# Performance work log

Hardware: AMD Instinct MI355X
Metric: run time of the kernel (lower is better)

## Reference

```python
import jax, jax.numpy as jnp
import numpy as np

N, C, E, K = 50000, 128, 640000, 40  # nodes, feat dim, edges, classes
EPS = 1e-5


def setup_inputs() -> dict:
    key = jax.random.key(0)
    ks = jax.random.split(key, 8)
    s = 1.0 / np.sqrt(C)
    return {
        "x": jax.random.normal(ks[0], (N, C), jnp.float32),
        "edge_index": jax.random.randint(ks[1], (2, E), 0, N, dtype=jnp.int32),
        "W_conv": jax.random.normal(ks[2], (C, C), jnp.float32) * s,
        "b_conv": jnp.zeros((C,), jnp.float32),
        "gamma": jnp.ones((C,), jnp.float32),
        "beta": jnp.zeros((C,), jnp.float32),
        "W_fc": jax.random.normal(ks[3], (C, K), jnp.float32) * s,
        "b_fc": jnp.zeros((K,), jnp.float32),
    }


def reference(x, edge_index, W_conv, b_conv, gamma, beta, W_fc, b_fc):
    n = x.shape[0]
    loops = jnp.arange(n, dtype=edge_index.dtype)
    src = jnp.concatenate([edge_index[0], loops])  # add self-loops (PyG default)
    dst = jnp.concatenate([edge_index[1], loops])
    # symmetric normalization: deg^{-1/2}[src] * deg^{-1/2}[dst]
    deg = jax.ops.segment_sum(jnp.ones_like(dst, jnp.float32), dst, num_segments=n)
    dinv = jax.lax.rsqrt(jnp.maximum(deg, 1.0))  # deg >= 1 with self-loops
    norm = dinv[src] * dinv[dst]  # [E+N]
    h = x @ W_conv  # [N, C] transform before propagate (GCNConv)
    agg = jax.ops.segment_sum(h[src] * norm[:, None], dst, num_segments=n) + b_conv
    a = jax.nn.relu(agg) * x  # dropout = identity (eval mode); elementwise mul with residual
    mu = jnp.mean(a, axis=-1, keepdims=True)
    var = jnp.mean((a - mu) ** 2, axis=-1, keepdims=True)
    ln = (a - mu) * jax.lax.rsqrt(var + EPS) * gamma + beta
    return (ln + x) @ W_fc + b_fc
```

## Files before the change

### kernel.cpp

```cpp
#include <hip/hip_runtime.h>

#define C_DIM 128
#define EPS 1e-5f
#define DEG_CAP 64

typedef __attribute__((ext_vector_type(8))) short short8;
typedef __attribute__((ext_vector_type(4))) float f32x4;

__device__ __forceinline__ unsigned bf16rn(float f) {
    unsigned u = __float_as_uint(f);
    return (u + 0x7fffu + ((u >> 16) & 1u)) >> 16;
}
__device__ __forceinline__ unsigned pack_bf16(float lo, float hi) {
    return bf16rn(lo) | (bf16rn(hi) << 16);
}
__device__ __forceinline__ float blo(unsigned u) { return __uint_as_float(u << 16); }
__device__ __forceinline__ float bhi(unsigned u) { return __uint_as_float(u & 0xffff0000u); }

#define NSCAT 1250

__global__ __launch_bounds__(256, 2) void fat(const float* __restrict__ x,
                                              const float* __restrict__ W,
                                              unsigned* __restrict__ hb,
                                              const float* __restrict__ Wfc,
                                              unsigned short* __restrict__ WT,
                                              const int* __restrict__ esrc,
                                              const int* __restrict__ edst,
                                              int* __restrict__ cnt,
                                              int* __restrict__ bsrc,
                                              int n, int e, int g1) {
    __shared__ float xT[64][132];
    __shared__ float ws[64][132];
    int b = blockIdx.x;
    int t = threadIdx.x;

    if (b < g1) {
        int r0 = b * 128;
        int w = t >> 6, lane = t & 63;
        int wr = (w >> 1) * 64, wc = (w & 1) * 64;
        int lr = (lane >> 3) * 8, lc = (lane & 7) * 8;
        float acc[8][8] = {};
        for (int kc = 0; kc < 128; kc += 64) {
            __syncthreads();
#pragma unroll
            for (int i = 0; i < 8; i++) {
                int idx = t + i * 256;
                int r = idx >> 4;
                int k4 = (idx & 15) << 2;
                float4 v = make_float4(0.f, 0.f, 0.f, 0.f);
                if (r0 + r < n) v = *(const float4*)&x[(long)(r0 + r) * C_DIM + kc + k4];
                xT[k4 + 0][r] = v.x; xT[k4 + 1][r] = v.y; xT[k4 + 2][r] = v.z; xT[k4 + 3][r] = v.w;
            }
#pragma unroll
            for (int i = 0; i < 8; i++) {
                int idx = t + i * 256;
                int k = idx >> 5;
                int c4 = (idx & 31) << 2;
                *(float4*)&ws[k][c4] = *(const float4*)&W[(long)(kc + k) * C_DIM + c4];
            }
            __syncthreads();
#pragma unroll 4
            for (int k = 0; k < 64; k++) {
                float a[8], bb[8];
                *(float4*)&a[0] = *(float4*)&xT[k][wr + lr];
                *(float4*)&a[4] = *(float4*)&xT[k][wr + lr + 4];
                *(float4*)&bb[0] = *(float4*)&ws[k][wc + lc];
                *(float4*)&bb[4] = *(float4*)&ws[k][wc + lc + 4];
#pragma unroll
                for (int i = 0; i < 8; i++)
#pragma unroll
                    for (int j = 0; j < 8; j++)
                        acc[i][j] += a[i] * bb[j];
            }
        }
#pragma unroll
        for (int i = 0; i < 8; i++) {
            int r = r0 + wr + lr + i;
            if (r < n) {
                uint4 p;
                p.x = pack_bf16(acc[i][0], acc[i][1]);
                p.y = pack_bf16(acc[i][2], acc[i][3]);
                p.z = pack_bf16(acc[i][4], acc[i][5]);
                p.w = pack_bf16(acc[i][6], acc[i][7]);
                *(uint4*)&hb[(long)r * 64 + ((wc + lc) >> 1)] = p;
            }
        }
    } else if (b == g1) {
        for (int tid = t; tid < 48 * 128; tid += 256) {
            int nc = tid >> 7;
            int k = tid & 127;
            float v = (nc < 40) ? Wfc[k * 40 + nc] : 0.f;
            WT[nc * 128 + k] = (unsigned short)bf16rn(v);
        }
    } else {
        int sb = b - g1 - 1;
        int i = sb * 256 + t;
        int j = i + NSCAT * 256;
        if (i < e) {
            int d0 = edst[i];
            int s0 = esrc[i];
            int d1 = -1, s1 = 0;
            if (j < e) { d1 = edst[j]; s1 = esrc[j]; }
            int p0 = atomicAdd(&cnt[d0], 1);
            int p1 = (d1 >= 0) ? atomicAdd(&cnt[d1], 1) : 0;
            if (p0 < DEG_CAP) bsrc[(long)d0 * DEG_CAP + p0] = s0;
            if (d1 >= 0 && p1 < DEG_CAP) bsrc[(long)d1 * DEG_CAP + p1] = s1;
        }
    }
}

__global__ __launch_bounds__(256) void aggregate(const unsigned* __restrict__ hb,
                                                 const float* __restrict__ x,
                                                 const int* __restrict__ cnt,
                                                 const int* __restrict__ bsrc,
                                                 const float* __restrict__ bconv,
                                                 const float* __restrict__ gamma,
                                                 const float* __restrict__ beta,
                                                 unsigned* __restrict__ zb, int n) {
    int wid = (blockIdx.x * blockDim.x + threadIdx.x) >> 6;
    if (wid >= n) return;
    int lane = threadIdx.x & 63;
    int sub = lane & 15, grp = lane >> 4;
    int i = wid;
    int degt = cnt[i];
    float di = rsqrtf((float)degt + 1.0f);
    int deg = degt > DEG_CAP ? DEG_CAP : degt;
    long base = (long)i * DEG_CAP;

    uint4 us = *(const uint4*)(hb + (long)i * 64 + sub * 4);
    float wself = (grp == 0) ? di * di : 0.f;
    float acc[8];
    acc[0] = wself * blo(us.x); acc[1] = wself * bhi(us.x);
    acc[2] = wself * blo(us.y); acc[3] = wself * bhi(us.y);
    acc[4] = wself * blo(us.z); acc[5] = wself * bhi(us.z);
    acc[6] = wself * blo(us.w); acc[7] = wself * bhi(us.w);

    int k = grp;
    for (; k + 4 < deg; k += 8) {
        int s0 = bsrc[base + k];
        int s1 = bsrc[base + k + 4];
        float w0 = rsqrtf((float)cnt[s0] + 1.0f) * di;
        float w1 = rsqrtf((float)cnt[s1] + 1.0f) * di;
        uint4 u0 = *(const uint4*)(hb + (long)s0 * 64 + sub * 4);
        uint4 u1 = *(const uint4*)(hb + (long)s1 * 64 + sub * 4);
        acc[0] += w0 * blo(u0.x); acc[1] += w0 * bhi(u0.x);
        acc[2] += w0 * blo(u0.y); acc[3] += w0 * bhi(u0.y);
        acc[4] += w0 * blo(u0.z); acc[5] += w0 * bhi(u0.z);
        acc[6] += w0 * blo(u0.w); acc[7] += w0 * bhi(u0.w);
        acc[0] += w1 * blo(u1.x); acc[1] += w1 * bhi(u1.x);
        acc[2] += w1 * blo(u1.y); acc[3] += w1 * bhi(u1.y);
        acc[4] += w1 * blo(u1.z); acc[5] += w1 * bhi(u1.z);
        acc[6] += w1 * blo(u1.w); acc[7] += w1 * bhi(u1.w);
    }
    for (; k < deg; k += 4) {
        int s = bsrc[base + k];
        float w = rsqrtf((float)cnt[s] + 1.0f) * di;
        uint4 u = *(const uint4*)(hb + (long)s * 64 + sub * 4);
        acc[0] += w * blo(u.x); acc[1] += w * bhi(u.x);
        acc[2] += w * blo(u.y); acc[3] += w * bhi(u.y);
        acc[4] += w * blo(u.z); acc[5] += w * bhi(u.z);
        acc[6] += w * blo(u.w); acc[7] += w * bhi(u.w);
    }

#pragma unroll
    for (int j = 0; j < 8; j++) {
        acc[j] += __shfl_xor(acc[j], 16);
        acc[j] += __shfl_xor(acc[j], 32);
    }

    float4 bca = *(const float4*)&bconv[sub * 8];
    float4 bcb = *(const float4*)&bconv[sub * 8 + 4];
    float4 xa  = *(const float4*)&x[(long)i * C_DIM + sub * 8];
    float4 xb  = *(const float4*)&x[(long)i * C_DIM + sub * 8 + 4];
    float a[8], xv[8];
    xv[0] = xa.x; xv[1] = xa.y; xv[2] = xa.z; xv[3] = xa.w;
    xv[4] = xb.x; xv[5] = xb.y; xv[6] = xb.z; xv[7] = xb.w;
    float bc[8] = {bca.x, bca.y, bca.z, bca.w, bcb.x, bcb.y, bcb.z, bcb.w};
#pragma unroll
    for (int j = 0; j < 8; j++) a[j] = fmaxf(acc[j] + bc[j], 0.f) * xv[j];

    float s = a[0] + a[1] + a[2] + a[3] + a[4] + a[5] + a[6] + a[7];
#pragma unroll
    for (int off = 1; off < 16; off <<= 1) s += __shfl_xor(s, off);
    float mu = s * (1.0f / 128.0f);
    float d[8], v = 0.f;
#pragma unroll
    for (int j = 0; j < 8; j++) { d[j] = a[j] - mu; v += d[j] * d[j]; }
#pragma unroll
    for (int off = 1; off < 16; off <<= 1) v += __shfl_xor(v, off);
    float inv = rsqrtf(v * (1.0f / 128.0f) + EPS);

    if (grp == 0) {
        float4 ga = *(const float4*)&gamma[sub * 8];
        float4 gb = *(const float4*)&gamma[sub * 8 + 4];
        float4 ba = *(const float4*)&beta[sub * 8];
        float4 bb = *(const float4*)&beta[sub * 8 + 4];
        float g[8] = {ga.x, ga.y, ga.z, ga.w, gb.x, gb.y, gb.z, gb.w};
        float be[8] = {ba.x, ba.y, ba.z, ba.w, bb.x, bb.y, bb.z, bb.w};
        float o[8];
#pragma unroll
        for (int j = 0; j < 8; j++) o[j] = d[j] * inv * g[j] + be[j] + xv[j];
        uint4 p;
        p.x = pack_bf16(o[0], o[1]);
        p.y = pack_bf16(o[2], o[3]);
        p.z = pack_bf16(o[4], o[5]);
        p.w = pack_bf16(o[6], o[7]);
        *(uint4*)(zb + (long)i * 64 + sub * 4) = p;
    }
}

__global__ __launch_bounds__(256) void gemm2(const unsigned short* __restrict__ zb,
                                             const unsigned short* __restrict__ WT,
                                             const float* __restrict__ bfc,
                                             float* __restrict__ out, int n) {
    int t = threadIdx.x;
    int w = t >> 6, lane = t & 63;
    int r0 = (blockIdx.x * 4 + w) * 64;
    if (r0 >= n) return;
    int mrow = lane & 15;
    int quad = lane >> 4;
    f32x4 acc[4][3];
#pragma unroll
    for (int m = 0; m < 4; m++)
#pragma unroll
        for (int nt = 0; nt < 3; nt++) acc[m][nt] = (f32x4){0.f, 0.f, 0.f, 0.f};
#pragma unroll
    for (int ks = 0; ks < 4; ks++) {
        short8 A[4], B[3];
#pragma unroll
        for (int m = 0; m < 4; m++) {
            int r = r0 + m * 16 + mrow;
            if (r >= n) r = n - 1;
            A[m] = *(const short8*)&zb[(long)r * 128 + ks * 32 + quad * 8];
        }
#pragma unroll
        for (int nt = 0; nt < 3; nt++)
            B[nt] = *(const short8*)&WT[(nt * 16 + mrow) * 128 + ks * 32 + quad * 8];
#pragma unroll
        for (int m = 0; m < 4; m++)
#pragma unroll
            for (int nt = 0; nt < 3; nt++)
                acc[m][nt] = __builtin_amdgcn_mfma_f32_16x16x32_bf16(A[m], B[nt], acc[m][nt], 0, 0, 0);
    }
#pragma unroll
    for (int nt = 0; nt < 3; nt++) {
        int c = nt * 16 + mrow;
        if (c < 40) {
            float bias = bfc[c];
#pragma unroll
            for (int m = 0; m < 4; m++) {
#pragma unroll
                for (int reg = 0; reg < 4; reg++) {
                    int r = r0 + m * 16 + quad * 4 + reg;
                    if (r < n) out[(long)r * 40 + c] = acc[m][nt][reg] + bias;
                }
            }
        }
    }
}

extern "C" void kernel_launch(void* const* d_in, const int* in_sizes, int n_in,
                              void* d_out, int out_size, void* d_ws, size_t ws_size,
                              hipStream_t stream) {
    const float* x     = (const float*)d_in[0];
    const int*   ei    = (const int*)d_in[1];
    const float* Wc    = (const float*)d_in[2];
    const float* bc    = (const float*)d_in[3];
    const float* gamma = (const float*)d_in[4];
    const float* beta  = (const float*)d_in[5];
    const float* Wfc   = (const float*)d_in[6];
    const float* bfc   = (const float*)d_in[7];
    float* out = (float*)d_out;

    int N = in_sizes[0] / C_DIM;
    int E = in_sizes[1] / 2;
    const int* esrc = ei;
    const int* edst = ei + E;

    char* p = (char*)d_ws;
    auto carve = [&](size_t bytes) {
        void* q = (void*)p;
        p += (bytes + 255) & ~(size_t)255;
        return q;
    };
    unsigned* hb       = (unsigned*)carve((size_t)N * 64 * 4);
    unsigned* zb       = (unsigned*)carve((size_t)N * 64 * 4);
    unsigned short* WT = (unsigned short*)carve(48 * 128 * 2);
    int*   cnt         = (int*)carve((size_t)N * 4);
    int*   bsrc        = (int*)carve((size_t)N * DEG_CAP * 4);

    (void)hipMemsetAsync(cnt, 0, (size_t)N * 4, stream);

    int g1 = (N + 127) / 128;
    fat<<<g1 + 1 + NSCAT, 256, 0, stream>>>(x, Wc, hb, Wfc, WT, esrc, edst, cnt, bsrc,
                                            N, E, g1);

    aggregate<<<((size_t)N * 64 + 255) / 256, 256, 0, stream>>>(
        hb, x, cnt, bsrc, bc, gamma, beta, zb, N);

    gemm2<<<(N / 64 + 4) / 4, 256, 0, stream>>>((const unsigned short*)zb, WT, bfc, out, N);
}
```

Measured before the change: 167.6 us.

## Use split-bf16 MFMA for conv GEMM, compact edge buckets, shuffle-broadcast neighbor weights

Replaces the fp32 LDS-tiled GEMM with MFMA bf16 instructions using a hi/lo split of x and W (three products) to keep near-fp32 accuracy. W is pre-split and transposed by a new prep kernel that also zeroes counters, replacing the memset. Edge buckets now store 16-bit source indices and use two counters filled from opposite ends to reduce atomic contention. The aggregate kernel loads all neighbor indices and normalization weights once per wave and broadcasts them via shuffles instead of reloading per iteration. The 16-bit indices assume fewer than 65536 nodes, and the kernel adds one extra launch.

```diff
diff --git a/kernel.cpp b/kernel.cpp
--- a/kernel.cpp
+++ b/kernel.cpp
@@ -2,7 +2,7 @@
 
 #define C_DIM 128
 #define EPS 1e-5f
-#define DEG_CAP 64
+#define NSCAT 1250
 
 typedef __attribute__((ext_vector_type(8))) short short8;
 typedef __attribute__((ext_vector_type(4))) float f32x4;
@@ -17,102 +17,119 @@
 __device__ __forceinline__ float blo(unsigned u) { return __uint_as_float(u << 16); }
 __device__ __forceinline__ float bhi(unsigned u) { return __uint_as_float(u & 0xffff0000u); }
 
-#define NSCAT 1250
-
-__global__ __launch_bounds__(256, 2) void fat(const float* __restrict__ x,
-                                              const float* __restrict__ W,
-                                              unsigned* __restrict__ hb,
-                                              const float* __restrict__ Wfc,
-                                              unsigned short* __restrict__ WT,
+__global__ void prep0(const float* __restrict__ W, const float* __restrict__ Wfc,
+                      unsigned short* __restrict__ WhT, unsigned short* __restrict__ WlT,
+                      unsigned short* __restrict__ WT,
+                      int* __restrict__ cntA, int* __restrict__ cntB, int n) {
+    int gid = blockIdx.x * blockDim.x + threadIdx.x;
+    int stride = gridDim.x * blockDim.x;
+    for (int t = gid; t < 128 * 128; t += stride) {
+        int c = t >> 7, k = t & 127;
+        float v = W[k * 128 + c];
+        unsigned hi = bf16rn(v);
+        float fh = __uint_as_float(hi << 16);
+        WhT[c * 128 + k] = (unsigned short)hi;
+        WlT[c * 128 + k] = (unsigned short)bf16rn(v - fh);
+    }
+    for (int t = gid; t < 48 * 128; t += stride) {
+        int nc = t >> 7, k = t & 127;
+        WT[nc * 128 + k] = (unsigned short)((nc < 40) ? bf16rn(Wfc[k * 40 + nc]) : 0u);
+    }
+    for (int t = gid; t < n; t += stride) {
+        cntA[t] = 0;
+        cntB[t] = 0;
+    }
+}
+
+__global__ __launch_bounds__(256, 4) void fat(const float* __restrict__ x,
+                                              const unsigned short* __restrict__ WhT,
+                                              const unsigned short* __restrict__ WlT,
+                                              unsigned short* __restrict__ hbs,
                                               const int* __restrict__ esrc,
                                               const int* __restrict__ edst,
-                                              int* __restrict__ cnt,
-                                              int* __restrict__ bsrc,
-                                              int n, int e, int g1) {
-    __shared__ float xT[64][132];
-    __shared__ float ws[64][132];
+                                              int* __restrict__ cntA,
+                                              int* __restrict__ cntB,
+                                              unsigned short* __restrict__ bsrcu,
+                                              int n, int e) {
     int b = blockIdx.x;
     int t = threadIdx.x;
 
-    if (b < g1) {
-        int r0 = b * 128;
-        int w = t >> 6, lane = t & 63;
-        int wr = (w >> 1) * 64, wc = (w & 1) * 64;
-        int lr = (lane >> 3) * 8, lc = (lane & 7) * 8;
-        float acc[8][8] = {};
-        for (int kc = 0; kc < 128; kc += 64) {
-            __syncthreads();
-#pragma unroll
-            for (int i = 0; i < 8; i++) {
-                int idx = t + i * 256;
-                int r = idx >> 4;
-                int k4 = (idx & 15) << 2;
-                float4 v = make_float4(0.f, 0.f, 0.f, 0.f);
-                if (r0 + r < n) v = *(const float4*)&x[(long)(r0 + r) * C_DIM + kc + k4];
-                xT[k4 + 0][r] = v.x; xT[k4 + 1][r] = v.y; xT[k4 + 2][r] = v.z; xT[k4 + 3][r] = v.w;
+    if (b < NSCAT) {
+        int half = NSCAT * 256;
+        int i = b * 256 + t;
+        int j = i + half;
+        if (i < e) {
+            int d0 = edst[i], s0 = esrc[i];
+            int p0 = atomicAdd(&cntA[d0], 1);
+            if (p0 < 64) bsrcu[(long)d0 * 64 + p0] = (unsigned short)s0;
+        }
+        if (j < e) {
+            int d1 = edst[j], s1 = esrc[j];
+            int p1 = atomicAdd(&cntB[d1], 1);
+            if (p1 < 64) bsrcu[(long)d1 * 64 + 63 - p1] = (unsigned short)s1;
+        }
+    } else {
+        int r0 = (b - NSCAT) * 128;
+        int wid = t >> 6, lane = t & 63;
+        int mrow = lane & 15, quad = lane >> 4;
+        int rb = r0 + wid * 32;
+
+        f32x4 acc[2][8];
+#pragma unroll
+        for (int m = 0; m < 2; m++)
+#pragma unroll
+            for (int nn = 0; nn < 8; nn++) acc[m][nn] = (f32x4){0.f, 0.f, 0.f, 0.f};
+
+#pragma unroll
+        for (int ks = 0; ks < 4; ks++) {
+            short8 Ah[2], Al[2];
+#pragma unroll
+            for (int m = 0; m < 2; m++) {
+                int r = rb + m * 16 + mrow;
+                if (r >= n) r = n - 1;
+                const float* xp = &x[(long)r * C_DIM + ks * 32 + quad * 8];
+                float4 va = *(const float4*)xp;
+                float4 vb = *(const float4*)(xp + 4);
+                float xv[8] = {va.x, va.y, va.z, va.w, vb.x, vb.y, vb.z, vb.w};
+#pragma unroll
+                for (int e8 = 0; e8 < 8; e8++) {
+                    unsigned hi = bf16rn(xv[e8]);
+                    Ah[m][e8] = (short)hi;
+                    Al[m][e8] = (short)bf16rn(xv[e8] - __uint_as_float(hi << 16));
+                }
             }
 #pragma unroll
-            for (int i = 0; i < 8; i++) {
-                int idx = t + i * 256;
-                int k = idx >> 5;
-                int c4 = (idx & 31) << 2;
-                *(float4*)&ws[k][c4] = *(const float4*)&W[(long)(kc + k) * C_DIM + c4];
+            for (int nn = 0; nn < 8; nn++) {
+                int wof = (nn * 16 + mrow) * 128 + ks * 32 + quad * 8;
+                short8 Bh = *(const short8*)&WhT[wof];
+                short8 Bl = *(const short8*)&WlT[wof];
+#pragma unroll
+                for (int m = 0; m < 2; m++) {
+                    acc[m][nn] = __builtin_amdgcn_mfma_f32_16x16x32_bf16(Ah[m], Bh, acc[m][nn], 0, 0, 0);
+                    acc[m][nn] = __builtin_amdgcn_mfma_f32_16x16x32_bf16(Al[m], Bh, acc[m][nn], 0, 0, 0);
+                    acc[m][nn] = __builtin_amdgcn_mfma_f32_16x16x32_bf16(Ah[m], Bl, acc[m][nn], 0, 0, 0);
+                }
             }
-            __syncthreads();
-#pragma unroll 4
-            for (int k = 0; k < 64; k++) {
-                float a[8], bb[8];
-                *(float4*)&a[0] = *(float4*)&xT[k][wr + lr];
-                *(float4*)&a[4] = *(float4*)&xT[k][wr + lr + 4];
-                *(float4*)&bb[0] = *(float4*)&ws[k][wc + lc];
-                *(float4*)&bb[4] = *(float4*)&ws[k][wc + lc + 4];
-#pragma unroll
-                for (int i = 0; i < 8; i++)
-#pragma unroll
-                    for (int j = 0; j < 8; j++)
-                        acc[i][j] += a[i] * bb[j];
+        }
+#pragma unroll
+        for (int m = 0; m < 2; m++)
+#pragma unroll
+            for (int nn = 0; nn < 8; nn++) {
+                int c = nn * 16 + mrow;
+#pragma unroll
+                for (int reg = 0; reg < 4; reg++) {
+                    int r = rb + m * 16 + quad * 4 + reg;
+                    if (r < n) hbs[(long)r * 128 + c] = (unsigned short)bf16rn(acc[m][nn][reg]);
+                }
             }
-        }
-#pragma unroll
-        for (int i = 0; i < 8; i++) {
-            int r = r0 + wr + lr + i;
-            if (r < n) {
-                uint4 p;
-                p.x = pack_bf16(acc[i][0], acc[i][1]);
-                p.y = pack_bf16(acc[i][2], acc[i][3]);
-                p.z = pack_bf16(acc[i][4], acc[i][5]);
-                p.w = pack_bf16(acc[i][6], acc[i][7]);
-                *(uint4*)&hb[(long)r * 64 + ((wc + lc) >> 1)] = p;
-            }
-        }
-    } else if (b == g1) {
-        for (int tid = t; tid < 48 * 128; tid += 256) {
-            int nc = tid >> 7;
-            int k = tid & 127;
-            float v = (nc < 40) ? Wfc[k * 40 + nc] : 0.f;
-            WT[nc * 128 + k] = (unsigned short)bf16rn(v);
-        }
-    } else {
-        int sb = b - g1 - 1;
-        int i = sb * 256 + t;
-        int j = i + NSCAT * 256;
-        if (i < e) {
-            int d0 = edst[i];
-            int s0 = esrc[i];
-            int d1 = -1, s1 = 0;
-            if (j < e) { d1 = edst[j]; s1 = esrc[j]; }
-            int p0 = atomicAdd(&cnt[d0], 1);
-            int p1 = (d1 >= 0) ? atomicAdd(&cnt[d1], 1) : 0;
-            if (p0 < DEG_CAP) bsrc[(long)d0 * DEG_CAP + p0] = s0;
-            if (d1 >= 0 && p1 < DEG_CAP) bsrc[(long)d1 * DEG_CAP + p1] = s1;
-        }
     }
 }
 
 __global__ __launch_bounds__(256) void aggregate(const unsigned* __restrict__ hb,
                                                  const float* __restrict__ x,
-                                                 const int* __restrict__ cnt,
-                                                 const int* __restrict__ bsrc,
+                                                 const int* __restrict__ cntA,
+                                                 const int* __restrict__ cntB,
+                                                 const unsigned short* __restrict__ bsrcu,
                                                  const float* __restrict__ bconv,
                                                  const float* __restrict__ gamma,
                                                  const float* __restrict__ beta,
@@ -122,10 +139,18 @@
     int lane = threadIdx.x & 63;
     int sub = lane & 15, grp = lane >> 4;
     int i = wid;
-    int degt = cnt[i];
-    float di = rsqrtf((float)degt + 1.0f);
-    int deg = degt > DEG_CAP ? DEG_CAP : degt;
-    long base = (long)i * DEG_CAP;
+
+    int dA = cntA[i], dB = cntB[i];
+    float di = rsqrtf((float)(dA + dB) + 1.0f);
+    if (dA > 64) dA = 64;
+    if (dB > 64 - dA) dB = 64 - dA;
+    int tot = dA + dB;
+    int shift = 64 - tot;
+
+    int sraw = (int)bsrcu[(long)i * 64 + lane];
+    bool valid = (lane < dA) | (lane >= 64 - dB);
+    int s_all = valid ? sraw : 0;
+    float w_all = valid ? rsqrtf((float)(cntA[s_all] + cntB[s_all]) + 1.0f) * di : 0.f;
 
     uint4 us = *(const uint4*)(hb + (long)i * 64 + sub * 4);
     float wself = (grp == 0) ? di * di : 0.f;
@@ -135,12 +160,18 @@
     acc[4] = wself * blo(us.z); acc[5] = wself * bhi(us.z);
     acc[6] = wself * blo(us.w); acc[7] = wself * bhi(us.w);
 
-    int k = grp;
-    for (; k + 4 < deg; k += 8) {
-        int s0 = bsrc[base + k];
-        int s1 = bsrc[base + k + 4];
-        float w0 = rsqrtf((float)cnt[s0] + 1.0f) * di;
-        float w1 = rsqrtf((float)cnt[s1] + 1.0f) * di;
+    int nIt = (tot + 7) >> 3;
+    for (int it = 0; it < nIt; ++it) {
+        int t0 = grp + it * 8;
+        int t1 = t0 + 4;
+        int sl0 = ((t0 < dA) ? t0 : t0 + shift) & 63;
+        int sl1 = ((t1 < dA) ? t1 : t1 + shift) & 63;
+        int s0 = __shfl(s_all, sl0);
+        float w0 = __shfl(w_all, sl0);
+        int s1 = __shfl(s_all, sl1);
+        float w1 = __shfl(w_all, sl1);
+        if (t0 >= tot) { w0 = 0.f; s0 = i; }
+        if (t1 >= tot) { w1 = 0.f; s1 = i; }
         uint4 u0 = *(const uint4*)(hb + (long)s0 * 64 + sub * 4);
         uint4 u1 = *(const uint4*)(hb + (long)s1 * 64 + sub * 4);
         acc[0] += w0 * blo(u0.x); acc[1] += w0 * bhi(u0.x);
@@ -151,15 +182,6 @@
         acc[2] += w1 * blo(u1.y); acc[3] += w1 * bhi(u1.y);
         acc[4] += w1 * blo(u1.z); acc[5] += w1 * bhi(u1.z);
         acc[6] += w1 * blo(u1.w); acc[7] += w1 * bhi(u1.w);
-    }
-    for (; k < deg; k += 4) {
-        int s = bsrc[base + k];
-        float w = rsqrtf((float)cnt[s] + 1.0f) * di;
-        uint4 u = *(const uint4*)(hb + (long)s * 64 + sub * 4);
-        acc[0] += w * blo(u.x); acc[1] += w * bhi(u.x);
-        acc[2] += w * blo(u.y); acc[3] += w * bhi(u.y);
-        acc[4] += w * blo(u.z); acc[5] += w * bhi(u.z);
-        acc[6] += w * blo(u.w); acc[7] += w * bhi(u.w);
     }
 
 #pragma unroll
@@ -283,20 +305,23 @@
         p += (bytes + 255) & ~(size_t)255;
         return q;
     };
-    unsigned* hb       = (unsigned*)carve((size_t)N * 64 * 4);
-    unsigned* zb       = (unsigned*)carve((size_t)N * 64 * 4);
-    unsigned short* WT = (unsigned short*)carve(48 * 128 * 2);
-    int*   cnt         = (int*)carve((size_t)N * 4);
-    int*   bsrc        = (int*)carve((size_t)N * DEG_CAP * 4);
-
-    (void)hipMemsetAsync(cnt, 0, (size_t)N * 4, stream);
+    unsigned* hb        = (unsigned*)carve((size_t)N * 64 * 4);
+    unsigned* zb        = (unsigned*)carve((size_t)N * 64 * 4);
+    unsigned short* WT  = (unsigned short*)carve(48 * 128 * 2);
+    unsigned short* WhT = (unsigned short*)carve(128 * 128 * 2);
+    unsigned short* WlT = (unsigned short*)carve(128 * 128 * 2);
+    int* cntA           = (int*)carve((size_t)N * 4);
+    int* cntB           = (int*)carve((size_t)N * 4);
+    unsigned short* bsrcu = (unsigned short*)carve((size_t)N * 64 * 2);
+
+    prep0<<<64, 256, 0, stream>>>(Wc, Wfc, WhT, WlT, WT, cntA, cntB, N);
 
     int g1 = (N + 127) / 128;
-    fat<<<g1 + 1 + NSCAT, 256, 0, stream>>>(x, Wc, hb, Wfc, WT, esrc, edst, cnt, bsrc,
-                                            N, E, g1);
+    fat<<<NSCAT + g1, 256, 0, stream>>>(x, WhT, WlT, (unsigned short*)hb, esrc, edst,
+                                        cntA, cntB, bsrcu, N, E);
 
     aggregate<<<((size_t)N * 64 + 255) / 256, 256, 0, stream>>>(
-        hb, x, cnt, bsrc, bc, gamma, beta, zb, N);
+        hb, x, cntA, cntB, bsrcu, bc, gamma, beta, zb, N);
 
     gemm2<<<(N / 64 + 4) / 4, 256, 0, stream>>>((const unsigned short*)zb, WT, bfc, out, N);
 }
```

Measured after the change: 206.5 us. 23.2% more time.
